# Kernel optimization log

Measured on AMD Instinct MI355X. Metric: run time of the kernel, lower is better.

## Reference

```python
import jax, jax.numpy as jnp
import numpy as np

L, D, H, DFF, DEP = 3, 256, 8, 1024, 40
B, S = 8, 512
DK = D // H
ALPHA, BETA = 1.0, 1.0
NEG = -1e18


def _ln(x, g, b, eps=1e-6):
    m = x.mean(-1, keepdims=True)
    v = ((x - m) ** 2).mean(-1, keepdims=True)
    return (x - m) / jnp.sqrt(v + eps) * g + b


def setup_inputs():
    key = jax.random.key(0)
    ks = jax.random.split(key, 16)
    g = lambda k, shape, s=0.02: jax.random.normal(k, shape, jnp.float32) * s
    return {
        "src": jax.random.normal(ks[0], (B, S, D), jnp.float32),
        "mask": jax.random.randint(ks[1], (B, S, S), 0, 2, dtype=jnp.int32),
        "key_padding_mask": jnp.ones((B, 1, S), jnp.int32),
        "structure": jax.random.normal(ks[2], (B, S, S, DEP), jnp.float32),
        "Wq": g(ks[3], (L, D, D)), "bq": jnp.zeros((L, D), jnp.float32),
        "Wk": g(ks[4], (L, D, D)), "bk": jnp.zeros((L, D), jnp.float32),
        "Wv": g(ks[5], (L, D, D)), "bv": jnp.zeros((L, D), jnp.float32),
        "Wo": g(ks[6], (L, D, D)), "bo": jnp.zeros((L, D), jnp.float32),
        "Wsk": g(ks[7], (L, DEP, DK)), "bsk": jnp.zeros((L, DK), jnp.float32),
        "Wsv": g(ks[8], (L, DEP, DK)), "bsv": jnp.zeros((L, DK), jnp.float32),
        "ln1_g": jnp.ones((L, D), jnp.float32), "ln1_b": jnp.zeros((L, D), jnp.float32),
        "Wf1": g(ks[9], (L, D, DFF)), "bf1": jnp.zeros((L, DFF), jnp.float32),
        "Wf2": g(ks[10], (L, DFF, D)), "bf2": jnp.zeros((L, D), jnp.float32),
        "lnf_g": jnp.ones((D,), jnp.float32), "lnf_b": jnp.zeros((D,), jnp.float32),
    }


def _layer(x, mask, kpm, structure, Wq, bq, Wk, bk, Wv, bv, Wo, bo,
           Wsk, bsk, Wsv, bsv, ln1_g, ln1_b, Wf1, bf1, Wf2, bf2):
    b, s, d = x.shape
    split = lambda t: t.reshape(b, s, H, DK).transpose(0, 2, 1, 3)  # [b,h,s,dk]
    q = split(x @ Wq + bq) / jnp.sqrt(jnp.float32(DK))
    k = split(x @ Wk + bk)
    v = split(x @ Wv + bv)
    scores = jnp.einsum("bhqd,bhkd->bhqk", q, k)
    # structure-aware bias: project dep-type embeddings to per-head key space
    sk = structure @ Wsk + bsk  # [b,q,k,dk]
    scores = scores + ALPHA * jnp.einsum("bhqd,bqkd->bhqk", q, sk)
    scores = jnp.where(mask[:, None, :, :] == 0, NEG, scores)      # adjacency mask
    scores = jnp.where(kpm[:, :, None, :] == 0, NEG, scores)       # key padding mask
    attn = jax.nn.softmax(scores, axis=-1)
    ctx = jnp.einsum("bhqk,bhkd->bhqd", attn, v)
    sv = structure @ Wsv + bsv  # [b,q,k,dk]
    ctx = ctx + BETA * jnp.einsum("bhqk,bqkd->bhqd", attn, sv)
    ctx = ctx.transpose(0, 2, 1, 3).reshape(b, s, d)
    out = (ctx @ Wo + bo) + x  # residual (dropout = identity in eval)
    # positionwise FFN (pre-norm OpenNMT style) with residual
    h = _ln(out, ln1_g, ln1_b)
    h = jax.nn.relu(h @ Wf1 + bf1)
    return (h @ Wf2 + bf2) + out


def reference(src, mask, key_padding_mask, structure, Wq, bq, Wk, bk, Wv, bv,
              Wo, bo, Wsk, bsk, Wsv, bsv, ln1_g, ln1_b, Wf1, bf1, Wf2, bf2,
              lnf_g, lnf_b):
    out = src
    for i in range(L):
        out = _layer(out, mask, key_padding_mask, structure,
                     Wq[i], bq[i], Wk[i], bk[i], Wv[i], bv[i], Wo[i], bo[i],
                     Wsk[i], bsk[i], Wsv[i], bsv[i], ln1_g[i], ln1_b[i],
                     Wf1[i], bf1[i], Wf2[i], bf2[i])
    return _ln(out, lnf_g, lnf_b)
```

## Files before the change

kernel.cpp:

```cpp
#include <hip/hip_runtime.h>
#include <hip/hip_bf16.h>
#include <math.h>

#define L_   3
#define D_   256
#define H_   8
#define DFF_ 1024
#define DEP_ 40
#define B_   8
#define S_   512
#define DK_  32
#define NEG_ (-1e18f)
#define TK3  32

typedef __attribute__((ext_vector_type(8))) short    s16x8;
typedef __attribute__((ext_vector_type(8))) _Float16 f16x8;
typedef __attribute__((ext_vector_type(4))) float    f32x4;

__device__ __forceinline__ short f2h(float f) {
    union { _Float16 h; short s; } u;
    u.h = (_Float16)f;
    return u.s;
}

__global__ void copy_kernel(const float4* __restrict__ in, float4* __restrict__ out, int n4) {
    int i = blockIdx.x * blockDim.x + threadIdx.x;
    if (i < n4) out[i] = in[i];
}

__device__ __forceinline__ float dot4(float4 a, float4 b) {
    return a.x * b.x + a.y * b.y + a.z * b.z + a.w * b.w;
}

__global__ __launch_bounds__(256)
void wconv(const float* __restrict__ in, short* __restrict__ out, int K, int N)
{
    __shared__ float t[32][33];
    const size_t l = blockIdx.z;
    in  += l * (size_t)K * N;
    out += l * (size_t)K * N;
    int n0 = blockIdx.x * 32, k0 = blockIdx.y * 32;
    int tx = threadIdx.x & 31, ty = threadIdx.x >> 5;
    #pragma unroll
    for (int r = 0; r < 32; r += 8)
        t[ty + r][tx] = in[(size_t)(k0 + ty + r) * N + n0 + tx];
    __syncthreads();
    #pragma unroll
    for (int r = 0; r < 32; r += 8)
        out[(size_t)(n0 + ty + r) * K + k0 + tx] = f2h(t[tx][ty + r]);
}

template<bool QKV, bool RELU, bool AHALF, bool OUTHF>
__global__ __launch_bounds__(256)
void gemm_mfma(const void* __restrict__ Ap,
               const short* __restrict__ W0, const short* __restrict__ W1,
               const short* __restrict__ W2,
               const float* __restrict__ b0, const float* __restrict__ b1,
               const float* __restrict__ b2,
               const float* __restrict__ resid,
               float* __restrict__ C0, float* __restrict__ C1,
               float* __restrict__ C2,
               short* __restrict__ Chf,
               int M, int N, int K, float scale)
{
    __shared__ short As[2][64 * 32];
    __shared__ short Bs[2][64 * 32];

    const int bm = blockIdx.y * 64;
    int bn = blockIdx.x * 64;
    int sel = 0;
    if (QKV) { sel = bn >> 8; bn &= 255; }
    const short* Wt   = QKV ? (sel == 0 ? W0 : (sel == 1 ? W1 : W2)) : W0;
    const float* bias = QKV ? (sel == 0 ? b0 : (sel == 1 ? b1 : b2)) : b0;
    float*       C    = QKV ? (sel == 0 ? C0 : (sel == 1 ? C1 : C2)) : C0;
    const float  scl  = (QKV && sel > 0) ? 1.f : scale;
    const int    ldc  = QKV ? 256 : N;

    const int tid  = threadIdx.x;
    const int row  = tid >> 2;
    const int kq   = (tid & 3) * 8;
    const int wid  = tid >> 6, lane = tid & 63;
    const int wm   = wid >> 1, wn = wid & 1;
    const int lr   = lane & 15, lk = (lane >> 4) * 8;

    const float* Af = (const float*)Ap;
    const short* Ah = (const short*)Ap;
    const size_t aoff = (size_t)(bm + row) * K + kq;
    const size_t boff = (size_t)(bn + row) * K + kq;
    const int    lofs = row * 32 + kq;

    f32x4 acc00 = {0.f, 0.f, 0.f, 0.f};
    f32x4 acc01 = acc00, acc10 = acc00, acc11 = acc00;

    {
        s16x8 ha;
        if (AHALF) {
            ha = *(const s16x8*)&Ah[aoff];
        } else {
            float4 p0 = *(const float4*)&Af[aoff];
            float4 p1 = *(const float4*)&Af[aoff + 4];
            ha[0] = f2h(p0.x); ha[1] = f2h(p0.y); ha[2] = f2h(p0.z); ha[3] = f2h(p0.w);
            ha[4] = f2h(p1.x); ha[5] = f2h(p1.y); ha[6] = f2h(p1.z); ha[7] = f2h(p1.w);
        }
        *(s16x8*)&As[0][lofs] = ha;
        *(s16x8*)&Bs[0][lofs] = *(const s16x8*)&Wt[boff];
    }

    const int nt = K >> 5;
    for (int t = 0; t < nt; ++t) {
        const int buf = t & 1;
        __syncthreads();
        float4 p0, p1; s16x8 ha, hb;
        const bool pf = (t + 1 < nt);
        if (pf) {
            const int k0 = (t + 1) << 5;
            if (AHALF) {
                ha = *(const s16x8*)&Ah[aoff + k0];
            } else {
                p0 = *(const float4*)&Af[aoff + k0];
                p1 = *(const float4*)&Af[aoff + k0 + 4];
            }
            hb = *(const s16x8*)&Wt[boff + k0];
        }
        f16x8 a0 = *(const f16x8*)&As[buf][(wm * 32 + lr) * 32 + lk];
        f16x8 a1 = *(const f16x8*)&As[buf][(wm * 32 + 16 + lr) * 32 + lk];
        f16x8 v0 = *(const f16x8*)&Bs[buf][(wn * 32 + lr) * 32 + lk];
        f16x8 v1 = *(const f16x8*)&Bs[buf][(wn * 32 + 16 + lr) * 32 + lk];
        acc00 = __builtin_amdgcn_mfma_f32_16x16x32_f16(a0, v0, acc00, 0, 0, 0);
        acc01 = __builtin_amdgcn_mfma_f32_16x16x32_f16(a0, v1, acc01, 0, 0, 0);
        acc10 = __builtin_amdgcn_mfma_f32_16x16x32_f16(a1, v0, acc10, 0, 0, 0);
        acc11 = __builtin_amdgcn_mfma_f32_16x16x32_f16(a1, v1, acc11, 0, 0, 0);
        if (pf) {
            if (!AHALF) {
                ha[0] = f2h(p0.x); ha[1] = f2h(p0.y); ha[2] = f2h(p0.z); ha[3] = f2h(p0.w);
                ha[4] = f2h(p1.x); ha[5] = f2h(p1.y); ha[6] = f2h(p1.z); ha[7] = f2h(p1.w);
            }
            *(s16x8*)&As[buf ^ 1][lofs] = ha;
            *(s16x8*)&Bs[buf ^ 1][lofs] = hb;
        }
    }

    f32x4 accs[2][2] = {{acc00, acc01}, {acc10, acc11}};
    #pragma unroll
    for (int fm = 0; fm < 2; ++fm) {
        #pragma unroll
        for (int fn = 0; fn < 2; ++fn) {
            #pragma unroll
            for (int j = 0; j < 4; ++j) {
                int m = bm + wm * 32 + fm * 16 + (lane >> 4) * 4 + j;
                int n = bn + wn * 32 + fn * 16 + lr;
                float v = (accs[fm][fn][j] + bias[n]) * scl;
                if (resid) v += resid[(size_t)m * ldc + n];
                if (RELU)  v = fmaxf(v, 0.f);
                if (OUTHF) Chf[(size_t)m * ldc + n] = f2h(v);
                else       C[(size_t)m * ldc + n]   = v;
            }
        }
    }
}

__global__ __launch_bounds__(256)
void attn_kernel(const float* __restrict__ qb,
                 const float* __restrict__ kb,
                 const float* __restrict__ vb,
                 const float* __restrict__ structure,
                 const int*   __restrict__ mask,
                 const int*   __restrict__ kpm,
                 const float* __restrict__ Wsk, const float* __restrict__ bsk,
                 const float* __restrict__ Wsv, const float* __restrict__ bsv,
                 float* __restrict__ ctx)
{
    __shared__ float q_s[D_];
    __shared__ float wqk_s[H_][44];
    __shared__ float hb_s[H_];
    __shared__ float st_s[2][TK3][44];
    __shared__ float dead_s[2][TK3];
    __shared__ float sc_s[H_][TK3];

    const int b   = blockIdx.x & 7;
    const int qi  = blockIdx.x >> 3;
    const int tid = threadIdx.x;
    const int h    = tid >> 5;
    const int lane = tid & 31;

    q_s[tid] = qb[((size_t)b * S_ + qi) * D_ + tid];
    __syncthreads();

    for (int p = tid; p < H_ * DEP_; p += 256) {
        int hh = p / DEP_, dep = p - hh * DEP_;
        const float4* wr = (const float4*)(Wsk + dep * DK_);
        const float4* qr = (const float4*)(q_s + hh * DK_);
        float s = 0.f;
        #pragma unroll
        for (int c = 0; c < 8; ++c) s += dot4(qr[c], wr[c]);
        wqk_s[hh][dep] = s;
    }
    if (tid < H_) {
        const float4* qr = (const float4*)(q_s + tid * DK_);
        const float4* br = (const float4*)bsk;
        float s = 0.f;
        #pragma unroll
        for (int c = 0; c < 8; ++c) s += dot4(qr[c], br[c]);
        hb_s[tid] = s;
    }
    __syncthreads();

    float4 wqk_r[10];
    #pragma unroll
    for (int c = 0; c < 10; ++c) wqk_r[c] = *(float4*)&wqk_s[h][c * 4];
    const float hb = hb_s[h];

    const float* kbase = kb + (size_t)b * S_ * D_;
    const float* vbase = vb + (size_t)b * S_ * D_ + tid;
    const float* strow = structure + (size_t)(b * S_ + qi) * S_ * DEP_;
    const int*   mrow  = mask + (size_t)(b * S_ + qi) * S_;
    const int*   krow  = kpm + (size_t)b * S_;

    for (int c = tid; c < TK3 * 10; c += 256) {
        int kk = c / 10, d4 = c - kk * 10;
        *(float4*)&st_s[0][kk][d4 * 4] =
            *(const float4*)&strow[(size_t)kk * DEP_ + d4 * 4];
    }
    if (tid < TK3) dead_s[0][tid] = (mrow[tid] == 0 || krow[tid] == 0) ? NEG_ : 0.f;

    float m_run = -INFINITY, l_run = 0.f, vacc = 0.f;
    float4 ps_r[10];
    #pragma unroll
    for (int c = 0; c < 10; ++c) ps_r[c] = make_float4(0.f, 0.f, 0.f, 0.f);

    const float4* qp = (const float4*)(q_s + h * DK_);

    for (int t = 0; t < S_ / TK3; ++t) {
        const int buf = t & 1;
        const int k0  = t * TK3;
        __syncthreads();
        if (t + 1 < S_ / TK3) {
            const int kn = k0 + TK3;
            for (int c = tid; c < TK3 * 10; c += 256) {
                int kk = c / 10, d4 = c - kk * 10;
                *(float4*)&st_s[buf ^ 1][kk][d4 * 4] =
                    *(const float4*)&strow[(size_t)(kn + kk) * DEP_ + d4 * 4];
            }
            if (tid < TK3)
                dead_s[buf ^ 1][tid] = (mrow[kn + tid] == 0 || krow[kn + tid] == 0) ? NEG_ : 0.f;
        }
        const int key = k0 + lane;
        const float4* kp = (const float4*)(kbase + (size_t)key * D_ + h * DK_);
        float kq = 0.f;
        #pragma unroll
        for (int c = 0; c < 8; ++c) kq += dot4(qp[c], kp[c]);
        const float4* sp = (const float4*)&st_s[buf][lane][0];
        float bias = hb;
        #pragma unroll
        for (int c = 0; c < 10; ++c) bias += dot4(sp[c], wqk_r[c]);
        float sc = kq + bias + dead_s[buf][lane];
        float tm = sc;
        #pragma unroll
        for (int off = 16; off; off >>= 1) tm = fmaxf(tm, __shfl_xor(tm, off));
        float m_new = fmaxf(m_run, tm);
        float e = __expf(sc - m_new);
        float psum = e;
        #pragma unroll
        for (int off = 16; off; off >>= 1) psum += __shfl_xor(psum, off);
        if (m_new > m_run) {
            float alpha = __expf(m_run - m_new);
            l_run *= alpha;
            vacc  *= alpha;
            #pragma unroll
            for (int c = 0; c < 10; ++c) {
                ps_r[c].x *= alpha; ps_r[c].y *= alpha;
                ps_r[c].z *= alpha; ps_r[c].w *= alpha;
            }
            m_run = m_new;
        }
        l_run += psum;
        sc_s[h][lane] = e;
        #pragma unroll
        for (int c = 0; c < 10; ++c) {
            float4 sv = sp[c];
            ps_r[c].x += e * sv.x;
            ps_r[c].y += e * sv.y;
            ps_r[c].z += e * sv.z;
            ps_r[c].w += e * sv.w;
        }
        #pragma unroll 8
        for (int k = 0; k < TK3; ++k) {
            vacc += sc_s[h][k] * vbase[(size_t)(k0 + k) * D_];
        }
    }

    float* pf = (float*)ps_r;
    #pragma unroll
    for (int j = 0; j < DEP_; ++j) {
        float v = pf[j];
        #pragma unroll
        for (int off = 16; off; off >>= 1) v += __shfl_xor(v, off);
        pf[j] = v;
    }
    float sv = 0.f;
    #pragma unroll
    for (int j = 0; j < DEP_; ++j) sv += pf[j] * Wsv[j * DK_ + lane];
    float invl = 1.f / l_run;
    ctx[((size_t)b * S_ + qi) * D_ + tid] = (vacc + sv) * invl + bsv[lane];
}

__global__ __launch_bounds__(256)
void ln_kernel(const float* __restrict__ x, const float* __restrict__ g,
               const float* __restrict__ b, float* __restrict__ out)
{
    int row = blockIdx.x, tid = threadIdx.x;
    float v = x[(size_t)row * D_ + tid];
    float s = v, ss = v * v;
    #pragma unroll
    for (int off = 32; off; off >>= 1) {
        s  += __shfl_xor(s, off);
        ss += __shfl_xor(ss, off);
    }
    __shared__ float rs[4], rss[4];
    int wid = tid >> 6, lane = tid & 63;
    if (lane == 0) { rs[wid] = s; rss[wid] = ss; }
    __syncthreads();
    float sum  = rs[0] + rs[1] + rs[2] + rs[3];
    float ssum = rss[0] + rss[1] + rss[2] + rss[3];
    float mean = sum * (1.f / D_);
    float var  = ssum * (1.f / D_) - mean * mean;
    out[(size_t)row * D_ + tid] = (v - mean) * rsqrtf(var + 1e-6f) * g[tid] + b[tid];
}

extern "C" void kernel_launch(void* const* d_in, const int* in_sizes, int n_in,
                              void* d_out, int out_size, void* d_ws, size_t ws_size,
                              hipStream_t stream)
{
    (void)in_sizes; (void)n_in; (void)out_size; (void)ws_size;
    const float* src       = (const float*)d_in[0];
    const int*   mask      = (const int*)  d_in[1];
    const int*   kpm       = (const int*)  d_in[2];
    const float* structure = (const float*)d_in[3];
    const float* Wq  = (const float*)d_in[4];  const float* bq  = (const float*)d_in[5];
    const float* Wk  = (const float*)d_in[6];  const float* bk  = (const float*)d_in[7];
    const float* Wv  = (const float*)d_in[8];  const float* bv  = (const float*)d_in[9];
    const float* Wo  = (const float*)d_in[10]; const float* bo  = (const float*)d_in[11];
    const float* Wsk = (const float*)d_in[12]; const float* bsk = (const float*)d_in[13];
    const float* Wsv = (const float*)d_in[14]; const float* bsv = (const float*)d_in[15];
    const float* ln1g = (const float*)d_in[16]; const float* ln1b = (const float*)d_in[17];
    const float* Wf1 = (const float*)d_in[18]; const float* bf1 = (const float*)d_in[19];
    const float* Wf2 = (const float*)d_in[20]; const float* bf2 = (const float*)d_in[21];
    const float* lnfg = (const float*)d_in[22]; const float* lnfb = (const float*)d_in[23];

    const int M = B_ * S_;
    const size_t NB = (size_t)M * D_;
    float* ws   = (float*)d_ws;
    float* x    = ws;
    float* qb   = ws + 1 * NB;
    float* kb2  = ws + 2 * NB;
    float* vb2  = ws + 3 * NB;
    float* ctx  = ws + 4 * NB;
    float* outb = ws + 5 * NB;
    float* hln  = ws + 6 * NB;
    short* f1hf = (short*)(ws + 7 * NB);
    short* wq_t  = (short*)(ws + 9 * NB);
    short* wk_t  = wq_t  + (size_t)L_ * D_ * D_;
    short* wv_t  = wk_t  + (size_t)L_ * D_ * D_;
    short* wo_t  = wv_t  + (size_t)L_ * D_ * D_;
    short* wf1_t = wo_t  + (size_t)L_ * D_ * D_;
    short* wf2_t = wf1_t + (size_t)L_ * D_ * DFF_;

    copy_kernel<<<1024, 256, 0, stream>>>((const float4*)src, (float4*)x, (int)(NB / 4));

    wconv<<<dim3(D_ / 32, D_ / 32, L_), 256, 0, stream>>>(Wq, wq_t, D_, D_);
    wconv<<<dim3(D_ / 32, D_ / 32, L_), 256, 0, stream>>>(Wk, wk_t, D_, D_);
    wconv<<<dim3(D_ / 32, D_ / 32, L_), 256, 0, stream>>>(Wv, wv_t, D_, D_);
    wconv<<<dim3(D_ / 32, D_ / 32, L_), 256, 0, stream>>>(Wo, wo_t, D_, D_);
    wconv<<<dim3(DFF_ / 32, D_ / 32, L_), 256, 0, stream>>>(Wf1, wf1_t, D_, DFF_);
    wconv<<<dim3(D_ / 32, DFF_ / 32, L_), 256, 0, stream>>>(Wf2, wf2_t, DFF_, D_);

    const float qscale = 0.17677669529663689f;
    for (int i = 0; i < L_; ++i) {
        const size_t od = (size_t)i * D_ * D_;
        const size_t of = (size_t)i * D_ * DFF_;
        gemm_mfma<true, false, false, false><<<dim3(12, 64), 256, 0, stream>>>(
            x, wq_t + od, wk_t + od, wv_t + od,
            bq + i * D_, bk + i * D_, bv + i * D_, nullptr,
            qb, kb2, vb2, nullptr, M, 768, D_, qscale);
        attn_kernel<<<B_ * S_, 256, 0, stream>>>(
            qb, kb2, vb2, structure, mask, kpm,
            Wsk + (size_t)i * DEP_ * DK_, bsk + i * DK_,
            Wsv + (size_t)i * DEP_ * DK_, bsv + i * DK_, ctx);
        gemm_mfma<false, false, false, false><<<dim3(4, 64), 256, 0, stream>>>(
            ctx, wo_t + od, wo_t + od, wo_t + od,
            bo + i * D_, nullptr, nullptr, x,
            outb, nullptr, nullptr, nullptr, M, D_, D_, 1.f);
        ln_kernel<<<M, 256, 0, stream>>>(outb, ln1g + i * D_, ln1b + i * D_, hln);
        gemm_mfma<false, true, false, true><<<dim3(16, 64), 256, 0, stream>>>(
            hln, wf1_t + of, wf1_t + of, wf1_t + of,
            bf1 + i * DFF_, nullptr, nullptr, nullptr,
            nullptr, nullptr, nullptr, f1hf, M, DFF_, D_, 1.f);
        gemm_mfma<false, false, true, false><<<dim3(4, 64), 256, 0, stream>>>(
            f1hf, wf2_t + of, wf2_t + of, wf2_t + of,
            bf2 + i * D_, nullptr, nullptr, outb,
            x, nullptr, nullptr, nullptr, M, D_, DFF_, 1.f);
    }
    ln_kernel<<<M, 256, 0, stream>>>(x, lnfg, lnfb, (float*)d_out);
}
```

Measured before the change: 2.303 ms.

## Prefetch structure tiles two steps ahead into registers with triple-buffered LDS

```diff
diff --git a/kernel.cpp b/kernel.cpp
--- a/kernel.cpp
+++ b/kernel.cpp
@@ -159,7 +159,7 @@
     }
 }
 
-__global__ __launch_bounds__(256)
+__global__ __launch_bounds__(256, 4)
 void attn_kernel(const float* __restrict__ qb,
                  const float* __restrict__ kb,
                  const float* __restrict__ vb,
@@ -173,8 +173,8 @@
     __shared__ float q_s[D_];
     __shared__ float wqk_s[H_][44];
     __shared__ float hb_s[H_];
-    __shared__ float st_s[2][TK3][44];
-    __shared__ float dead_s[2][TK3];
+    __shared__ float st_s[3][TK3][44];
+    __shared__ float dead_s[3][TK3];
     __shared__ float sc_s[H_][TK3];
 
     const int b   = blockIdx.x & 7;
@@ -205,44 +205,66 @@
     }
     __syncthreads();
 
-    float4 wqk_r[10];
-    #pragma unroll
-    for (int c = 0; c < 10; ++c) wqk_r[c] = *(float4*)&wqk_s[h][c * 4];
-    const float hb = hb_s[h];
-
     const float* kbase = kb + (size_t)b * S_ * D_;
     const float* vbase = vb + (size_t)b * S_ * D_ + tid;
     const float* strow = structure + (size_t)(b * S_ + qi) * S_ * DEP_;
     const int*   mrow  = mask + (size_t)(b * S_ + qi) * S_;
     const int*   krow  = kpm + (size_t)b * S_;
 
-    for (int c = tid; c < TK3 * 10; c += 256) {
-        int kk = c / 10, d4 = c - kk * 10;
-        *(float4*)&st_s[0][kk][d4 * 4] =
-            *(const float4*)&strow[(size_t)kk * DEP_ + d4 * 4];
-    }
-    if (tid < TK3) dead_s[0][tid] = (mrow[tid] == 0 || krow[tid] == 0) ? NEG_ : 0.f;
+    const int kk0 = tid / 10, d40 = tid - kk0 * 10;
+    const int c1  = tid + 256;
+    const int kk1 = c1 / 10,  d41 = c1 - kk1 * 10;
+    const bool has2 = (tid < 64);
+
+    const int nt = S_ / TK3;
+
+    {
+        *(f32x4*)&st_s[0][kk0][d40 * 4] =
+            __builtin_nontemporal_load((const f32x4*)&strow[(size_t)kk0 * DEP_ + d40 * 4]);
+        if (has2)
+            *(f32x4*)&st_s[0][kk1][d41 * 4] =
+                __builtin_nontemporal_load((const f32x4*)&strow[(size_t)kk1 * DEP_ + d41 * 4]);
+        if (tid < TK3)
+            dead_s[0][tid] =
+                (__builtin_nontemporal_load(&mrow[tid]) == 0 || krow[tid] == 0) ? NEG_ : 0.f;
+    }
+    f32x4 r1a = {0.f, 0.f, 0.f, 0.f}, r1b = r1a;
+    int m1 = 1, p1 = 1;
+    {
+        const float* s1 = strow + (size_t)TK3 * DEP_;
+        r1a = __builtin_nontemporal_load((const f32x4*)&s1[(size_t)kk0 * DEP_ + d40 * 4]);
+        if (has2) r1b = __builtin_nontemporal_load((const f32x4*)&s1[(size_t)kk1 * DEP_ + d41 * 4]);
+        if (tid < TK3) { m1 = __builtin_nontemporal_load(&mrow[TK3 + tid]); p1 = krow[TK3 + tid]; }
+    }
 
     float m_run = -INFINITY, l_run = 0.f, vacc = 0.f;
     float4 ps_r[10];
     #pragma unroll
     for (int c = 0; c < 10; ++c) ps_r[c] = make_float4(0.f, 0.f, 0.f, 0.f);
 
-    const float4* qp = (const float4*)(q_s + h * DK_);
-
-    for (int t = 0; t < S_ / TK3; ++t) {
-        const int buf = t & 1;
+    const float4* qp  = (const float4*)(q_s + h * DK_);
+    const float4* wq4 = (const float4*)&wqk_s[h][0];
+
+    for (int t = 0; t < nt; ++t) {
+        const int buf = t % 3;
         const int k0  = t * TK3;
         __syncthreads();
-        if (t + 1 < S_ / TK3) {
-            const int kn = k0 + TK3;
-            for (int c = tid; c < TK3 * 10; c += 256) {
-                int kk = c / 10, d4 = c - kk * 10;
-                *(float4*)&st_s[buf ^ 1][kk][d4 * 4] =
-                    *(const float4*)&strow[(size_t)(kn + kk) * DEP_ + d4 * 4];
+        f32x4 r2a = {0.f, 0.f, 0.f, 0.f}, r2b = r2a;
+        int m2 = 1, p2 = 1;
+        if (t + 2 < nt) {
+            const float* s2 = strow + (size_t)(t + 2) * TK3 * DEP_;
+            r2a = __builtin_nontemporal_load((const f32x4*)&s2[(size_t)kk0 * DEP_ + d40 * 4]);
+            if (has2) r2b = __builtin_nontemporal_load((const f32x4*)&s2[(size_t)kk1 * DEP_ + d41 * 4]);
+            if (tid < TK3) {
+                m2 = __builtin_nontemporal_load(&mrow[(t + 2) * TK3 + tid]);
+                p2 = krow[(t + 2) * TK3 + tid];
             }
-            if (tid < TK3)
-                dead_s[buf ^ 1][tid] = (mrow[kn + tid] == 0 || krow[kn + tid] == 0) ? NEG_ : 0.f;
+        }
+        if (t + 1 < nt) {
+            const int wb = (t + 1) % 3;
+            *(f32x4*)&st_s[wb][kk0][d40 * 4] = r1a;
+            if (has2) *(f32x4*)&st_s[wb][kk1][d41 * 4] = r1b;
+            if (tid < TK3) dead_s[wb][tid] = (m1 == 0 || p1 == 0) ? NEG_ : 0.f;
         }
         const int key = k0 + lane;
         const float4* kp = (const float4*)(kbase + (size_t)key * D_ + h * DK_);
@@ -250,9 +272,9 @@
         #pragma unroll
         for (int c = 0; c < 8; ++c) kq += dot4(qp[c], kp[c]);
         const float4* sp = (const float4*)&st_s[buf][lane][0];
-        float bias = hb;
-        #pragma unroll
-        for (int c = 0; c < 10; ++c) bias += dot4(sp[c], wqk_r[c]);
+        float bias = hb_s[h];
+        #pragma unroll
+        for (int c = 0; c < 10; ++c) bias += dot4(sp[c], wq4[c]);
         float sc = kq + bias + dead_s[buf][lane];
         float tm = sc;
         #pragma unroll
@@ -287,6 +309,7 @@
         for (int k = 0; k < TK3; ++k) {
             vacc += sc_s[h][k] * vbase[(size_t)(k0 + k) * D_];
         }
+        r1a = r2a; r1b = r2b; m1 = m2; p1 = p2;
     }
 
     float* pf = (float*)ps_r;
```

Measured after the change: 3.939 ms. 1.71x slower.
